# Kernel optimization log

Measured on AMD Instinct MI355X. Metric: run time of the kernel, lower is better.

## Reference

```python
import jax, jax.numpy as jnp
import numpy as np

EMBED = 768
HEAD = 256

def setup_inputs() -> dict:
    key = jax.random.key(0)
    k1, k2, k3, k4 = jax.random.split(key, 4)
    res_stream = jax.random.normal(k1, (512, 128, EMBED), dtype=jnp.float32)
    # torch Linear(embed, head, bias=False): y = x @ W.T, W: [head, embed].
    # Store as [embed, head] so y = x @ W.
    Wk = jax.random.normal(k2, (EMBED, HEAD), dtype=jnp.float32) * (EMBED ** -0.5)
    Wq = jax.random.normal(k3, (EMBED, HEAD), dtype=jnp.float32) * (EMBED ** -0.5)
    Wv = jax.random.normal(k4, (EMBED, HEAD), dtype=jnp.float32) * (EMBED ** -0.5)
    return {"res_stream": res_stream, "Wk": Wk, "Wq": Wq, "Wv": Wv}

def reference(res_stream, Wk, Wq, Wv):
    B, T, E = res_stream.shape
    q = jnp.einsum('bte,eh->bth', res_stream, Wq)  # [B,T,H]
    k = jnp.einsum('bte,eh->bth', res_stream, Wk)
    v = jnp.einsum('bte,eh->bth', res_stream, Wv)
    # NOTE: original scales by embed**-0.5 (not head_size**-0.5)
    scores = jnp.einsum('bth,bsh->bts', q, k) * (E ** -0.5)  # [B,T,T]
    causal = jnp.tril(jnp.ones((T, T), dtype=bool))
    scores = jnp.where(causal, scores, -jnp.inf)
    attn = jax.nn.softmax(scores, axis=-1)
    # dropout: eval mode (identity) for deterministic reference
    return jnp.einsum('bts,bsh->bth', attn, v)  # [B,T,H]
```

## Files before the change

### kernel.cpp

```cpp
#include <hip/hip_runtime.h>
#include <hip/hip_bf16.h>

typedef float f32x4 __attribute__((ext_vector_type(4)));
typedef short bfx8 __attribute__((ext_vector_type(8)));

typedef const __attribute__((address_space(1))) void* gvp;
typedef __attribute__((address_space(3))) void* lvp;

static __device__ __forceinline__ unsigned short f2bf(float f) {
    return __builtin_bit_cast(unsigned short, __float2bfloat16(f));
}

static __device__ __forceinline__ bfx8 cvt8(f32x4 lo, f32x4 hi) {
    bfx8 r;
    r[0] = (short)f2bf(lo[0]); r[1] = (short)f2bf(lo[1]);
    r[2] = (short)f2bf(lo[2]); r[3] = (short)f2bf(lo[3]);
    r[4] = (short)f2bf(hi[0]); r[5] = (short)f2bf(hi[1]);
    r[6] = (short)f2bf(hi[2]); r[7] = (short)f2bf(hi[3]);
    return r;
}

__global__ void prep_w(const float* __restrict__ Wk, const float* __restrict__ Wq,
                       const float* __restrict__ Wv, unsigned short* __restrict__ WT) {
    const int n = blockIdx.x;
    const int e = threadIdx.x;
    const int which = n >> 8;
    const int h = n & 255;
    const float* W = (which == 0) ? Wq : (which == 1) ? Wk : Wv;
    WT[(size_t)n * 768 + e] = f2bf(W[(size_t)e * 256 + h]);
}

__global__ __launch_bounds__(256) void qkv_gemm(const float* __restrict__ X,
                                                const unsigned short* __restrict__ WT,
                                                unsigned short* __restrict__ QKV) {
    __shared__ float          Abf[128][64];
    __shared__ unsigned short Bb[128][64];

    const int tid = threadIdx.x;
    const int bid = blockIdx.x;
    const int l   = (bid & 7) * 384 + (bid >> 3);
    const int bn  = l % 6;
    const int bm  = l / 6;
    const int m0 = bm * 128;
    const int n0 = bn * 128;
    const int w = tid >> 6, lane = tid & 63;
    const int wr = w >> 1, wc = w & 1;
    const int lrow = lane & 15, lhi = lane >> 4;
    const bool vswap = (bn >= 4);

    f32x4 acc[4][4];
    const f32x4 zero = {0.f, 0.f, 0.f, 0.f};
#pragma unroll
    for (int i = 0; i < 4; ++i)
#pragma unroll
        for (int j = 0; j < 4; ++j) acc[i][j] = zero;

    for (int kt = 0; kt < 12; ++kt) {
        const int k0 = kt * 64;
#pragma unroll
        for (int i = 0; i < 8; ++i) {
            const int f = i * 256 + tid;
            const int row = f >> 4;
            const int cb  = (f & 15) * 16;
            const int cbs = cb ^ ((row & 7) << 4);
            const float* g = X + (size_t)(m0 + row) * 768 + k0 + (cbs >> 2);
            char* lp = (char*)&Abf[0][0] + i * 4096 + w * 1024;
            __builtin_amdgcn_global_load_lds((gvp)g, (lvp)lp, 16, 0, 0);
        }
#pragma unroll
        for (int i = 0; i < 4; ++i) {
            const int f = i * 256 + tid;
            const int row = f >> 3;
            const int cb  = (f & 7) * 16;
            const int cbs = cb ^ ((row & 7) << 4);
            const unsigned short* g = WT + (size_t)(n0 + row) * 768 + k0 + (cbs >> 1);
            char* lp = (char*)&Bb[0][0] + i * 4096 + w * 1024;
            __builtin_amdgcn_global_load_lds((gvp)g, (lvp)lp, 16, 0, 0);
        }
        asm volatile("s_waitcnt vmcnt(0)" ::: "memory");
        __syncthreads();

#pragma unroll
        for (int kk = 0; kk < 2; ++kk) {
            const int kb = kk * 32 + lhi * 8;
            bfx8 a[4], bb4[4];
#pragma unroll
            for (int mi = 0; mi < 4; ++mi) {
                const int arow = wr * 64 + mi * 16 + lrow;
                const int s = (arow & 7) << 4;
                const char* ab = (const char*)&Abf[arow][0];
                f32x4 lo = *(const f32x4*)(ab + (((kb << 2))      ^ s));
                f32x4 hi = *(const f32x4*)(ab + (((kb << 2) + 16) ^ s));
                a[mi] = cvt8(lo, hi);
            }
#pragma unroll
            for (int ni = 0; ni < 4; ++ni) {
                const int brow = wc * 64 + ni * 16 + lrow;
                const int s = (brow & 7) << 4;
                const char* bb = (const char*)&Bb[brow][0];
                bb4[ni] = *(const bfx8*)(bb + ((kb << 1) ^ s));
            }
            if (!vswap) {
#pragma unroll
                for (int mi = 0; mi < 4; ++mi)
#pragma unroll
                    for (int ni = 0; ni < 4; ++ni)
                        acc[mi][ni] = __builtin_amdgcn_mfma_f32_16x16x32_bf16(
                            a[mi], bb4[ni], acc[mi][ni], 0, 0, 0);
            } else {
#pragma unroll
                for (int ni = 0; ni < 4; ++ni)
#pragma unroll
                    for (int mi = 0; mi < 4; ++mi)
                        acc[ni][mi] = __builtin_amdgcn_mfma_f32_16x16x32_bf16(
                            bb4[ni], a[mi], acc[ni][mi], 0, 0, 0);
            }
        }
        __syncthreads();
    }

    const int b = bm;
    if (!vswap) {
        const int which = bn >> 1;
        const size_t base = ((size_t)(b * 3 + which)) << 15;
        const int hbase = (bn & 1) * 128;
#pragma unroll
        for (int mi = 0; mi < 4; ++mi)
#pragma unroll
            for (int ni = 0; ni < 4; ++ni) {
                const int t = wr * 64 + mi * 16 + lhi * 4;
                const int h = hbase + wc * 64 + ni * 16 + lrow;
#pragma unroll
                for (int j = 0; j < 4; ++j)
                    QKV[base + (size_t)(t + j) * 256 + h] = f2bf(acc[mi][ni][j]);
            }
    } else {
        const size_t base = ((size_t)(b * 3 + 2)) << 15;
#pragma unroll
        for (int ni = 0; ni < 4; ++ni)
#pragma unroll
            for (int mi = 0; mi < 4; ++mi) {
                const int h = (bn - 4) * 128 + wc * 64 + ni * 16 + lhi * 4;
                const int t = wr * 64 + mi * 16 + lrow;
#pragma unroll
                for (int j = 0; j < 4; ++j)
                    QKV[base + (size_t)(h + j) * 128 + t] = f2bf(acc[ni][mi][j]);
            }
    }
}

__global__ __launch_bounds__(512) void attn(const unsigned short* __restrict__ QKV,
                                            float* __restrict__ Out) {
    __shared__ unsigned short Kl[128][264];
    __shared__ unsigned short Vt[256][136];

    const int b = blockIdx.x;
    const int tid = threadIdx.x;
    const int w = tid >> 6, lane = tid & 63;
    const int lrow = lane & 15, lhi = lane >> 4;

    const unsigned short* Qb = QKV + ((size_t)(b * 3 + 0) << 15);
    const unsigned short* Kb = QKV + ((size_t)(b * 3 + 1) << 15);
    const unsigned short* Vb = QKV + ((size_t)(b * 3 + 2) << 15);

    const int t0 = w * 16;
    bfx8 aq[8];
#pragma unroll
    for (int kk = 0; kk < 8; ++kk)
        aq[kk] = *(const bfx8*)(Qb + (size_t)(t0 + lrow) * 256 + kk * 32 + lhi * 8);

#pragma unroll
    for (int i = 0; i < 8; ++i) {
        int f = i * 512 + tid;
        {
            int row = f >> 5, c = (f & 31) * 8;
            *(bfx8*)&Kl[row][c] = *(const bfx8*)(Kb + (size_t)row * 256 + c);
        }
        {
            int row = f >> 4, c = (f & 15) * 8;
            *(bfx8*)&Vt[row][c] = *(const bfx8*)(Vb + (size_t)row * 128 + c);
        }
    }
    __syncthreads();

    f32x4 sacc[8];
    const f32x4 zero = {0.f, 0.f, 0.f, 0.f};
#pragma unroll
    for (int sj = 0; sj < 8; ++sj) sacc[sj] = zero;
#pragma unroll
    for (int kk = 0; kk < 8; ++kk) {
        const int kb = kk * 32 + lhi * 8;
#pragma unroll
        for (int sj = 0; sj < 8; ++sj) {
            bfx8 bk = *(const bfx8*)&Kl[sj * 16 + lrow][kb];
            sacc[sj] = __builtin_amdgcn_mfma_f32_16x16x32_bf16(aq[kk], bk, sacc[sj], 0, 0, 0);
        }
    }

    const float scale = 0.03608439182435161f;
    float inv[4];
#pragma unroll
    for (int j = 0; j < 4; ++j) {
        const int t = t0 + lhi * 4 + j;
        float m = -1e30f;
#pragma unroll
        for (int sj = 0; sj < 8; ++sj) {
            int s = sj * 16 + lrow;
            float vv = sacc[sj][j] * scale;
            vv = (s <= t) ? vv : -1e30f;
            sacc[sj][j] = vv;
            m = fmaxf(m, vv);
        }
#pragma unroll
        for (int d = 1; d < 16; d <<= 1) m = fmaxf(m, __shfl_xor(m, d));
        float sum = 0.f;
#pragma unroll
        for (int sj = 0; sj < 8; ++sj) {
            float e = __expf(sacc[sj][j] - m);
            sacc[sj][j] = e;
            sum += e;
        }
#pragma unroll
        for (int d = 1; d < 16; d <<= 1) sum += __shfl_xor(sum, d);
        inv[j] = 1.0f / sum;
    }

    __syncthreads();

    unsigned short* Pl = &Kl[0][0] + (size_t)w * (16 * 136);
#pragma unroll
    for (int sj = 0; sj < 8; ++sj)
#pragma unroll
        for (int j = 0; j < 4; ++j)
            Pl[(lhi * 4 + j) * 136 + sj * 16 + lrow] = f2bf(sacc[sj][j] * inv[j]);

    bfx8 pa[4];
#pragma unroll
    for (int kk = 0; kk < 4; ++kk)
        pa[kk] = *(const bfx8*)(Pl + lrow * 136 + kk * 32 + lhi * 8);

    f32x4 oacc[16];
#pragma unroll
    for (int ni = 0; ni < 16; ++ni) oacc[ni] = zero;
#pragma unroll
    for (int ni = 0; ni < 16; ++ni) {
#pragma unroll
        for (int kk = 0; kk < 4; ++kk) {
            bfx8 bv = *(const bfx8*)&Vt[ni * 16 + lrow][kk * 32 + lhi * 8];
            oacc[ni] = __builtin_amdgcn_mfma_f32_16x16x32_bf16(pa[kk], bv, oacc[ni], 0, 0, 0);
        }
    }

    float* Ob = Out + (size_t)b * 128 * 256;
#pragma unroll
    for (int ni = 0; ni < 16; ++ni) {
#pragma unroll
        for (int j = 0; j < 4; ++j) {
            const int t = t0 + lhi * 4 + j;
            const int h = ni * 16 + lrow;
            Ob[(size_t)t * 256 + h] = oacc[ni][j];
        }
    }
}

extern "C" void kernel_launch(void* const* d_in, const int* in_sizes, int n_in,
                              void* d_out, int out_size, void* d_ws, size_t ws_size,
                              hipStream_t stream) {
    (void)in_sizes; (void)n_in; (void)out_size; (void)ws_size;
    const float* X  = (const float*)d_in[0];
    const float* Wk = (const float*)d_in[1];
    const float* Wq = (const float*)d_in[2];
    const float* Wv = (const float*)d_in[3];

    unsigned short* WT  = (unsigned short*)d_ws;
    unsigned short* QKV = WT + (size_t)768 * 768;
    float* Out = (float*)d_out;

    prep_w<<<768, 768, 0, stream>>>(Wk, Wq, Wv, WT);
    qkv_gemm<<<3072, 256, 0, stream>>>(X, WT, QKV);
    attn<<<512, 512, 0, stream>>>(QKV, Out);
}
```

Measured before the change: 194.5 us.

## Load fp32 A operand directly into registers and double-buffer B tiles in LDS

The QKV GEMM no longer stages the fp32 activation tile through shared memory. Each wave reads its A rows straight from global memory into registers and converts them to bf16 there. The bf16 weight tile is double-buffered in LDS, so the next k-tile is prefetched with global_load_lds while the current one is consumed. This removes the large fp32 LDS staging and one barrier per iteration. The costs are that the two column-waves now fetch the same A rows twice from cache, and A-load latency sits unprefetched inside the MFMA loop. The explicit vmcnt wait before the barrier was dropped, so LDS-DMA completion ordering relies on the compiler.

```diff
diff --git a/kernel.cpp b/kernel.cpp
--- a/kernel.cpp
+++ b/kernel.cpp
@@ -33,8 +33,7 @@
 __global__ __launch_bounds__(256) void qkv_gemm(const float* __restrict__ X,
                                                 const unsigned short* __restrict__ WT,
                                                 unsigned short* __restrict__ QKV) {
-    __shared__ float          Abf[128][64];
-    __shared__ unsigned short Bb[128][64];
+    __shared__ unsigned short Bb[2][128][64];
 
     const int tid = threadIdx.x;
     const int bid = blockIdx.x;
@@ -55,50 +54,50 @@
 #pragma unroll
         for (int j = 0; j < 4; ++j) acc[i][j] = zero;
 
+    const float* Arow[4];
+#pragma unroll
+    for (int mi = 0; mi < 4; ++mi)
+        Arow[mi] = X + (size_t)(m0 + wr * 64 + mi * 16 + lrow) * 768;
+
+#define STAGE_B(kt, bs)                                                        \
+    {                                                                          \
+        const int k0s = (kt) * 64;                                             \
+        _Pragma("unroll")                                                      \
+        for (int i = 0; i < 4; ++i) {                                          \
+            const int f = i * 256 + tid;                                       \
+            const int row = f >> 3;                                            \
+            const int cb  = (f & 7) * 16;                                      \
+            const int cbs = cb ^ ((row & 7) << 4);                             \
+            const unsigned short* g = WT + (size_t)(n0 + row) * 768 + k0s + (cbs >> 1); \
+            char* lp = (char*)&Bb[bs][0][0] + i * 4096 + w * 1024;             \
+            __builtin_amdgcn_global_load_lds((gvp)g, (lvp)lp, 16, 0, 0);       \
+        }                                                                      \
+    }
+
+    STAGE_B(0, 0);
+    __syncthreads();
+
+    int cur = 0;
     for (int kt = 0; kt < 12; ++kt) {
+        if (kt < 11) STAGE_B(kt + 1, cur ^ 1);
         const int k0 = kt * 64;
-#pragma unroll
-        for (int i = 0; i < 8; ++i) {
-            const int f = i * 256 + tid;
-            const int row = f >> 4;
-            const int cb  = (f & 15) * 16;
-            const int cbs = cb ^ ((row & 7) << 4);
-            const float* g = X + (size_t)(m0 + row) * 768 + k0 + (cbs >> 2);
-            char* lp = (char*)&Abf[0][0] + i * 4096 + w * 1024;
-            __builtin_amdgcn_global_load_lds((gvp)g, (lvp)lp, 16, 0, 0);
-        }
-#pragma unroll
-        for (int i = 0; i < 4; ++i) {
-            const int f = i * 256 + tid;
-            const int row = f >> 3;
-            const int cb  = (f & 7) * 16;
-            const int cbs = cb ^ ((row & 7) << 4);
-            const unsigned short* g = WT + (size_t)(n0 + row) * 768 + k0 + (cbs >> 1);
-            char* lp = (char*)&Bb[0][0] + i * 4096 + w * 1024;
-            __builtin_amdgcn_global_load_lds((gvp)g, (lvp)lp, 16, 0, 0);
-        }
-        asm volatile("s_waitcnt vmcnt(0)" ::: "memory");
-        __syncthreads();
-
 #pragma unroll
         for (int kk = 0; kk < 2; ++kk) {
             const int kb = kk * 32 + lhi * 8;
             bfx8 a[4], bb4[4];
 #pragma unroll
-            for (int mi = 0; mi < 4; ++mi) {
-                const int arow = wr * 64 + mi * 16 + lrow;
-                const int s = (arow & 7) << 4;
-                const char* ab = (const char*)&Abf[arow][0];
-                f32x4 lo = *(const f32x4*)(ab + (((kb << 2))      ^ s));
-                f32x4 hi = *(const f32x4*)(ab + (((kb << 2) + 16) ^ s));
-                a[mi] = cvt8(lo, hi);
-            }
-#pragma unroll
             for (int ni = 0; ni < 4; ++ni) {
                 const int brow = wc * 64 + ni * 16 + lrow;
                 const int s = (brow & 7) << 4;
-                const char* bb = (const char*)&Bb[brow][0];
-                bb4[ni] = *(const bfx8*)(bb + ((kb << 1) ^ s));
+                const char* bp = (const char*)&Bb[cur][brow][0];
+                bb4[ni] = *(const bfx8*)(bp + ((kb << 1) ^ s));
+            }
+#pragma unroll
+            for (int mi = 0; mi < 4; ++mi) {
+                const float* p = Arow[mi] + k0 + kb;
+                f32x4 lo = *(const f32x4*)(p);
+                f32x4 hi = *(const f32x4*)(p + 4);
+                a[mi] = cvt8(lo, hi);
             }
             if (!vswap) {
 #pragma unroll
@@ -117,6 +116,7 @@
             }
         }
         __syncthreads();
+        cur ^= 1;
     }
 
     const int b = bm;
```

Measured after the change: 346.0 us. +77.9%, slower.
